# Kernel optimization log

Hardware: AMD Instinct MI355X
Metric: run time of the kernel (lower is better)

The kernel has to match this reference:

```python
import jax, jax.numpy as jnp
import numpy as np

NUM_LEARNERS = 50000
NUM_SCENES = 2000
EMBED_DIM = 128
SPARSITY = 0.1


def setup_inputs() -> dict:
    key = jax.random.key(0)
    k_m, k_w1, k_b1, k_w2, k_b2 = jax.random.split(key, 5)
    m = jax.random.uniform(k_m, (NUM_LEARNERS, NUM_SCENES), dtype=jnp.float32)
    m = jnp.where(m < SPARSITY, m, 0.0)
    return {
        "normalized_matrix": m,
        "W1": jax.random.normal(k_w1, (1, 16), dtype=jnp.float32),
        "b1": jax.random.normal(k_b1, (16,), dtype=jnp.float32),
        "W2": jax.random.normal(k_w2, (16, EMBED_DIM), dtype=jnp.float32),
        "b2": jax.random.normal(k_b2, (EMBED_DIM,), dtype=jnp.float32),
    }


def reference(normalized_matrix, W1, b1, W2, b2):
    # The torch module feeds the nonzero COLUMN INDICES (as floats) of each row
    # into MLP(1->16->d) and mean-pools. Since the MLP input is just the index j,
    # precompute mlp_out[j] for all scenes once, then a masked matmul + count
    # division gives the per-row mean over nonzero positions.
    num_scenes = normalized_matrix.shape[1]
    idx = jnp.arange(num_scenes, dtype=normalized_matrix.dtype)[:, None]  # [S, 1]
    h = jax.nn.relu(idx @ W1 + b1)                                        # [S, 16]
    mlp_out = h @ W2 + b2                                                 # [S, d]

    mask = (normalized_matrix != 0).astype(normalized_matrix.dtype)       # [L, S]
    counts = mask.sum(axis=1, keepdims=True)                              # [L, 1]
    # rows with zero nonzeros yield an all-zero mask row -> zero embedding,
    # matching the torch zeros fallback; clamp denominator to avoid 0/0.
    emb = (mask @ mlp_out) / jnp.maximum(counts, 1.0)                     # [L, d]
    return emb
```

## Files before the change

### kernel.cpp

```cpp
#include <hip/hip_runtime.h>
#include <hip/hip_fp16.h>

#define NUM_LEARNERS 50000
#define NUM_SCENES   2000
#define EMBED_DIM    128

typedef _Float16 half2v __attribute__((ext_vector_type(2)));

__global__ __launch_bounds__(256) void mlp_table_kernel(
    const float* __restrict__ W1, const float* __restrict__ b1,
    const float* __restrict__ W2, const float* __restrict__ b2,
    _Float16* __restrict__ mlp)
{
    int t = blockIdx.x * 256 + threadIdx.x;
    if (t >= NUM_SCENES * EMBED_DIM) return;
    int j = t >> 7;
    int d = t & 127;
    float x = (float)j;
    float acc = b2[d];
#pragma unroll
    for (int k = 0; k < 16; ++k) {
        float h = fmaf(x, W1[k], b1[k]);
        h = fmaxf(h, 0.0f);
        acc = fmaf(h, W2[k * EMBED_DIM + d], acc);
    }
    mlp[t] = (_Float16)acc;
}

__global__ __launch_bounds__(256) void gather_mean_kernel(
    const float* __restrict__ M, const _Float16* __restrict__ mlp,
    float* __restrict__ out)
{
    __shared__ unsigned short idxbuf[4][NUM_SCENES];
    const int  wave = threadIdx.x >> 6;
    const int  lane = threadIdx.x & 63;
    const long row  = (long)blockIdx.x * 4 + wave;

    const float4* __restrict__ M4 = (const float4*)(M + row * NUM_SCENES);
    unsigned short* myidx = idxbuf[wave];

    int count = 0;
    const unsigned long long below = (1ull << lane) - 1ull;
#pragma unroll
    for (int it = 0; it < 8; ++it) {
        int c4 = it * 64 + lane;
        float4 v = make_float4(0.f, 0.f, 0.f, 0.f);
        if (c4 < 500) v = M4[c4];
        float vals[4] = {v.x, v.y, v.z, v.w};
#pragma unroll
        for (int c = 0; c < 4; ++c) {
            bool nz = (vals[c] != 0.0f);
            unsigned long long m = __ballot(nz);
            if (nz) {
                int pos = count + __popcll(m & below);
                myidx[pos] = (unsigned short)(c4 * 4 + c);
            }
            count += __popcll(m);
        }
    }

    float ax = 0.f, ay = 0.f;
    const half2v* __restrict__ mlp2 = (const half2v*)mlp;
    const int base2 = lane;
#pragma unroll 4
    for (int n = 0; n < count; ++n) {
        int j = myidx[n];
        half2v p = mlp2[j * 64 + base2];
        ax += (float)p.x;
        ay += (float)p.y;
    }

    float inv = 1.0f / (float)(count > 0 ? count : 1);
    float2 r = make_float2(ax * inv, ay * inv);
    ((float2*)out)[row * 64 + lane] = r;
}

extern "C" void kernel_launch(void* const* d_in, const int* in_sizes, int n_in,
                              void* d_out, int out_size, void* d_ws, size_t ws_size,
                              hipStream_t stream) {
    const float* M  = (const float*)d_in[0];
    const float* W1 = (const float*)d_in[1];
    const float* b1 = (const float*)d_in[2];
    const float* W2 = (const float*)d_in[3];
    const float* b2 = (const float*)d_in[4];
    float* out = (float*)d_out;

    _Float16* mlp = (_Float16*)d_ws;

    mlp_table_kernel<<<(NUM_SCENES * EMBED_DIM + 255) / 256, 256, 0, stream>>>(
        W1, b1, W2, b2, mlp);
    gather_mean_kernel<<<NUM_LEARNERS / 4, 256, 0, stream>>>(M, mlp, out);
}
```

Before: 634.0 us.

## Pool 16-wide hidden activations before W2 instead of gathering 128-wide MLP outputs

Uses linearity of the second MLP layer: each row now sums the 16-dim ReLU hidden vectors over its nonzero columns, then applies W2 and count*b2 once per row. The per-nonzero gather shrinks from a 128-wide fp16 row to a 16-wide fp32 row, and 16 indices are processed in parallel per wave, followed by a shuffle reduction. It also switches to mbcnt for the prefix count. The kernel is likely bound by reading M (400MB), so the gain may be limited to the gather phase. A __syncthreads is added, and fp32 accumulation changes rounding slightly.

```diff
diff --git a/kernel.cpp b/kernel.cpp
--- a/kernel.cpp
+++ b/kernel.cpp
@@ -1,34 +1,24 @@
 #include <hip/hip_runtime.h>
-#include <hip/hip_fp16.h>
 
 #define NUM_LEARNERS 50000
 #define NUM_SCENES   2000
 #define EMBED_DIM    128
+#define HID          16
 
-typedef _Float16 half2v __attribute__((ext_vector_type(2)));
-
-__global__ __launch_bounds__(256) void mlp_table_kernel(
+__global__ __launch_bounds__(256) void h_table_kernel(
     const float* __restrict__ W1, const float* __restrict__ b1,
-    const float* __restrict__ W2, const float* __restrict__ b2,
-    _Float16* __restrict__ mlp)
+    float* __restrict__ htab)
 {
     int t = blockIdx.x * 256 + threadIdx.x;
-    if (t >= NUM_SCENES * EMBED_DIM) return;
-    int j = t >> 7;
-    int d = t & 127;
-    float x = (float)j;
-    float acc = b2[d];
-#pragma unroll
-    for (int k = 0; k < 16; ++k) {
-        float h = fmaf(x, W1[k], b1[k]);
-        h = fmaxf(h, 0.0f);
-        acc = fmaf(h, W2[k * EMBED_DIM + d], acc);
-    }
-    mlp[t] = (_Float16)acc;
+    if (t >= NUM_SCENES * HID) return;
+    int j = t >> 4;
+    int k = t & 15;
+    htab[t] = fmaxf(fmaf((float)j, W1[k], b1[k]), 0.0f);
 }
 
 __global__ __launch_bounds__(256) void gather_mean_kernel(
-    const float* __restrict__ M, const _Float16* __restrict__ mlp,
+    const float* __restrict__ M, const float* __restrict__ htab,
+    const float* __restrict__ W2, const float* __restrict__ b2,
     float* __restrict__ out)
 {
     __shared__ unsigned short idxbuf[4][NUM_SCENES];
@@ -40,7 +30,6 @@
     unsigned short* myidx = idxbuf[wave];
 
     int count = 0;
-    const unsigned long long below = (1ull << lane) - 1ull;
 #pragma unroll
     for (int it = 0; it < 8; ++it) {
         int c4 = it * 64 + lane;
@@ -52,27 +41,60 @@
             bool nz = (vals[c] != 0.0f);
             unsigned long long m = __ballot(nz);
             if (nz) {
-                int pos = count + __popcll(m & below);
-                myidx[pos] = (unsigned short)(c4 * 4 + c);
+                int below = __builtin_amdgcn_mbcnt_hi(
+                    (unsigned)(m >> 32),
+                    __builtin_amdgcn_mbcnt_lo((unsigned)m, 0));
+                myidx[count + below] = (unsigned short)(c4 * 4 + c);
             }
             count += __popcll(m);
         }
     }
 
-    float ax = 0.f, ay = 0.f;
-    const half2v* __restrict__ mlp2 = (const half2v*)mlp;
-    const int base2 = lane;
-#pragma unroll 4
-    for (int n = 0; n < count; ++n) {
-        int j = myidx[n];
-        half2v p = mlp2[j * 64 + base2];
-        ax += (float)p.x;
-        ay += (float)p.y;
+    __syncthreads();
+
+    const int g   = lane >> 2;
+    const int sub = lane & 3;
+    const float4* __restrict__ T4 = (const float4*)htab;
+
+    float4 acc = make_float4(0.f, 0.f, 0.f, 0.f);
+    for (int n = 0; n < count; n += 16) {
+        int i = n + g;
+        if (i < count) {
+            int j = myidx[i];
+            float4 v = T4[j * 4 + sub];
+            acc.x += v.x; acc.y += v.y; acc.z += v.z; acc.w += v.w;
+        }
     }
 
-    float inv = 1.0f / (float)(count > 0 ? count : 1);
-    float2 r = make_float2(ax * inv, ay * inv);
-    ((float2*)out)[row * 64 + lane] = r;
+#pragma unroll
+    for (int off = 4; off < 64; off <<= 1) {
+        acc.x += __shfl_xor(acc.x, off);
+        acc.y += __shfl_xor(acc.y, off);
+        acc.z += __shfl_xor(acc.z, off);
+        acc.w += __shfl_xor(acc.w, off);
+    }
+    float s[HID];
+#pragma unroll
+    for (int a = 0; a < 4; ++a) {
+        s[4 * a + 0] = __shfl(acc.x, a);
+        s[4 * a + 1] = __shfl(acc.y, a);
+        s[4 * a + 2] = __shfl(acc.z, a);
+        s[4 * a + 3] = __shfl(acc.w, a);
+    }
+
+    const float cnt = (float)count;
+    const float inv = 1.0f / fmaxf(cnt, 1.0f);
+    const float2* __restrict__ W2v = (const float2*)W2;
+    float2 bv = ((const float2*)b2)[lane];
+    float e0 = cnt * bv.x;
+    float e1 = cnt * bv.y;
+#pragma unroll
+    for (int k = 0; k < HID; ++k) {
+        float2 w = W2v[k * 64 + lane];
+        e0 = fmaf(s[k], w.x, e0);
+        e1 = fmaf(s[k], w.y, e1);
+    }
+    ((float2*)out)[row * 64 + lane] = make_float2(e0 * inv, e1 * inv);
 }
 
 extern "C" void kernel_launch(void* const* d_in, const int* in_sizes, int n_in,
@@ -85,9 +107,8 @@
     const float* b2 = (const float*)d_in[4];
     float* out = (float*)d_out;
 
-    _Float16* mlp = (_Float16*)d_ws;
+    float* htab = (float*)d_ws;
 
-    mlp_table_kernel<<<(NUM_SCENES * EMBED_DIM + 255) / 256, 256, 0, stream>>>(
-        W1, b1, W2, b2, mlp);
-    gather_mean_kernel<<<NUM_LEARNERS / 4, 256, 0, stream>>>(M, mlp, out);
+    h_table_kernel<<<(NUM_SCENES * HID + 255) / 256, 256, 0, stream>>>(W1, b1, htab);
+    gather_mean_kernel<<<NUM_LEARNERS / 4, 256, 0, stream>>>(M, htab, W2, b2, out);
 }
```

Result: faster. 564.8 us (-10.9%).

## Replace per-row sparse gather with dense masked GEMM on MFMA units

Applied to the files above, without the earlier changes.

Drops the ballot-based nonzero index compaction and the serial per-row gather of MLP table entries. Instead, each tile of the input is turned into a 0/1 fp16 mask in shared memory and multiplied against a transposed, zero-padded fp16 MLP table using 16x16x32 MFMA instructions, with register prefetch of the next K tile. Row counts are accumulated alongside and reduced with shuffles for the mean. This trades roughly ten times more arithmetic, since zeros are processed densely, for a streaming, bandwidth-bound access pattern. It also removes the latency-bound dependent loads in the gather loop.

```diff
diff --git a/kernel.cpp b/kernel.cpp
--- a/kernel.cpp
+++ b/kernel.cpp
@@ -1,78 +1,151 @@
 #include <hip/hip_runtime.h>
-#include <hip/hip_fp16.h>
 
-#define NUM_LEARNERS 50000
-#define NUM_SCENES   2000
-#define EMBED_DIM    128
+#define L  50000
+#define S  2000
+#define SP 2048
+#define D  128
+#define HID 16
+#define BM 64
+#define BK 64
+#define KITERS 32
 
-typedef _Float16 half2v __attribute__((ext_vector_type(2)));
+typedef _Float16 f16;
+typedef _Float16 half8  __attribute__((ext_vector_type(8)));
+typedef float    floatx4 __attribute__((ext_vector_type(4)));
 
-__global__ __launch_bounds__(256) void mlp_table_kernel(
+__global__ __launch_bounds__(256) void table_kernel(
     const float* __restrict__ W1, const float* __restrict__ b1,
     const float* __restrict__ W2, const float* __restrict__ b2,
-    _Float16* __restrict__ mlp)
+    f16* __restrict__ Bt)
 {
     int t = blockIdx.x * 256 + threadIdx.x;
-    if (t >= NUM_SCENES * EMBED_DIM) return;
-    int j = t >> 7;
-    int d = t & 127;
+    int d = t >> 11;
+    int j = t & 2047;
+    float acc = b2[d];
     float x = (float)j;
-    float acc = b2[d];
 #pragma unroll
-    for (int k = 0; k < 16; ++k) {
-        float h = fmaf(x, W1[k], b1[k]);
-        h = fmaxf(h, 0.0f);
-        acc = fmaf(h, W2[k * EMBED_DIM + d], acc);
+    for (int k = 0; k < HID; ++k) {
+        float h = fmaxf(fmaf(x, W1[k], b1[k]), 0.0f);
+        acc = fmaf(h, W2[k * D + d], acc);
     }
-    mlp[t] = (_Float16)acc;
+    Bt[t] = (j < S) ? (f16)acc : (f16)0.0f;
 }
 
-__global__ __launch_bounds__(256) void gather_mean_kernel(
-    const float* __restrict__ M, const _Float16* __restrict__ mlp,
+__global__ __launch_bounds__(256) void gemm_mask_kernel(
+    const float* __restrict__ M, const f16* __restrict__ Bt,
     float* __restrict__ out)
 {
-    __shared__ unsigned short idxbuf[4][NUM_SCENES];
-    const int  wave = threadIdx.x >> 6;
-    const int  lane = threadIdx.x & 63;
-    const long row  = (long)blockIdx.x * 4 + wave;
+    __shared__ f16  As[BM][72];
+    __shared__ f16  Bs[D][72];
+    __shared__ float cnt_s[BM];
 
-    const float4* __restrict__ M4 = (const float4*)(M + row * NUM_SCENES);
-    unsigned short* myidx = idxbuf[wave];
+    const int tid  = threadIdx.x;
+    const int wave = tid >> 6;
+    const int lane = tid & 63;
+    const long r0  = (long)blockIdx.x * BM;
 
-    int count = 0;
-    const unsigned long long below = (1ull << lane) - 1ull;
+    const int arow = tid >> 4;
+    const int acol = (tid & 15) * 4;
+    const int bd   = tid >> 1;
+    const int bko  = (tid & 1) * 32;
+
+    int cnt4[4] = {0, 0, 0, 0};
+    floatx4 acc[8];
 #pragma unroll
-    for (int it = 0; it < 8; ++it) {
-        int c4 = it * 64 + lane;
-        float4 v = make_float4(0.f, 0.f, 0.f, 0.f);
-        if (c4 < 500) v = M4[c4];
-        float vals[4] = {v.x, v.y, v.z, v.w};
+    for (int n = 0; n < 8; ++n) acc[n] = (floatx4){0.f, 0.f, 0.f, 0.f};
+
+    float4 av[4];
+    uint4  bv[4];
+    {
+        const int k0 = 0;
 #pragma unroll
-        for (int c = 0; c < 4; ++c) {
-            bool nz = (vals[c] != 0.0f);
-            unsigned long long m = __ballot(nz);
-            if (nz) {
-                int pos = count + __popcll(m & below);
-                myidx[pos] = (unsigned short)(c4 * 4 + c);
+        for (int p = 0; p < 4; ++p) {
+            long rg = r0 + p * 16 + arow;
+            bool ok = (rg < L);
+            av[p] = ok ? *(const float4*)(M + rg * S + k0 + acol)
+                       : make_float4(0.f, 0.f, 0.f, 0.f);
+        }
+#pragma unroll
+        for (int i = 0; i < 4; ++i)
+            bv[i] = *(const uint4*)(Bt + bd * SP + k0 + bko + i * 8);
+    }
+
+    for (int it = 0; it < KITERS; ++it) {
+        __syncthreads();
+
+#pragma unroll
+        for (int p = 0; p < 4; ++p) {
+            float4 v = av[p];
+            unsigned m0 = (v.x != 0.f) ? 0x3C00u : 0u;
+            unsigned m1 = (v.y != 0.f) ? 0x3C00u : 0u;
+            unsigned m2 = (v.z != 0.f) ? 0x3C00u : 0u;
+            unsigned m3 = (v.w != 0.f) ? 0x3C00u : 0u;
+            cnt4[p] += (v.x != 0.f) + (v.y != 0.f) + (v.z != 0.f) + (v.w != 0.f);
+            uint2 w;
+            w.x = m0 | (m1 << 16);
+            w.y = m2 | (m3 << 16);
+            *(uint2*)&As[p * 16 + arow][acol] = w;
+        }
+#pragma unroll
+        for (int i = 0; i < 4; ++i)
+            *(uint4*)&Bs[bd][bko + i * 8] = bv[i];
+
+        __syncthreads();
+
+        if (it + 1 < KITERS) {
+            const int k0 = (it + 1) * BK;
+#pragma unroll
+            for (int p = 0; p < 4; ++p) {
+                long rg = r0 + p * 16 + arow;
+                bool ok = (rg < L) && (k0 + acol < S);
+                av[p] = ok ? *(const float4*)(M + rg * S + k0 + acol)
+                           : make_float4(0.f, 0.f, 0.f, 0.f);
             }
-            count += __popcll(m);
+#pragma unroll
+            for (int i = 0; i < 4; ++i)
+                bv[i] = *(const uint4*)(Bt + bd * SP + k0 + bko + i * 8);
+        }
+
+#pragma unroll
+        for (int ks = 0; ks < 2; ++ks) {
+            half8 af = *(const half8*)&As[wave * 16 + (lane & 15)]
+                                         [(lane >> 4) * 8 + ks * 32];
+#pragma unroll
+            for (int n = 0; n < 8; ++n) {
+                half8 bf = *(const half8*)&Bs[n * 16 + (lane & 15)]
+                                             [(lane >> 4) * 8 + ks * 32];
+                acc[n] = __builtin_amdgcn_mfma_f32_16x16x32_f16(af, bf, acc[n], 0, 0, 0);
+            }
         }
     }
 
-    float ax = 0.f, ay = 0.f;
-    const half2v* __restrict__ mlp2 = (const half2v*)mlp;
-    const int base2 = lane;
-#pragma unroll 4
-    for (int n = 0; n < count; ++n) {
-        int j = myidx[n];
-        half2v p = mlp2[j * 64 + base2];
-        ax += (float)p.x;
-        ay += (float)p.y;
+#pragma unroll
+    for (int p = 0; p < 4; ++p) {
+        int c = cnt4[p];
+        c += __shfl_xor(c, 1);
+        c += __shfl_xor(c, 2);
+        c += __shfl_xor(c, 4);
+        c += __shfl_xor(c, 8);
+        if ((lane & 15) == 0)
+            cnt_s[p * 16 + wave * 4 + (lane >> 4)] = (float)c;
     }
+    __syncthreads();
 
-    float inv = 1.0f / (float)(count > 0 ? count : 1);
-    float2 r = make_float2(ax * inv, ay * inv);
-    ((float2*)out)[row * 64 + lane] = r;
+    float inv[4];
+#pragma unroll
+    for (int r = 0; r < 4; ++r) {
+        float c = cnt_s[wave * 16 + (lane >> 4) * 4 + r];
+        inv[r] = 1.0f / fmaxf(c, 1.0f);
+    }
+#pragma unroll
+    for (int n = 0; n < 8; ++n) {
+#pragma unroll
+        for (int r = 0; r < 4; ++r) {
+            long rg = r0 + wave * 16 + (lane >> 4) * 4 + r;
+            if (rg < L)
+                out[rg * D + n * 16 + (lane & 15)] = acc[n][r] * inv[r];
+        }
+    }
 }
 
 extern "C" void kernel_launch(void* const* d_in, const int* in_sizes, int n_in,
@@ -85,9 +158,8 @@
     const float* b2 = (const float*)d_in[4];
     float* out = (float*)d_out;
 
-    _Float16* mlp = (_Float16*)d_ws;
+    f16* Bt = (f16*)d_ws;
 
-    mlp_table_kernel<<<(NUM_SCENES * EMBED_DIM + 255) / 256, 256, 0, stream>>>(
-        W1, b1, W2, b2, mlp);
-    gather_mean_kernel<<<NUM_LEARNERS / 4, 256, 0, stream>>>(M, mlp, out);
+    table_kernel<<<(D * SP) / 256, 256, 0, stream>>>(W1, b1, W2, b2, Bt);
+    gemm_mask_kernel<<<(L + BM - 1) / BM, 256, 0, stream>>>(M, Bt, out);
 }
```

Result: slower. 703.2 us (+10.9%).

## Replace sparse gather-mean with dense MFMA masked GEMM against transposed table

Applied to the files above, without the earlier changes.

Replaces the per-row nonzero index compaction and gather loop with a dense masked matmul. The binary mask is built on the fly from the fp32 input as fp16 ones and multiplied against a transposed, padded fp16 MLP table using 16x16x32 MFMA instructions, with next-step A loads prefetched. This removes the ballot and LDS compaction work and the irregular gathers, but does the full dense 2000-wide reduction per row instead of only the roughly 10% nonzeros. It relies on reading the table from cache and on the input read being the dominant cost. Output stores are strided per lane and may coalesce less well.

```diff
diff --git a/kernel.cpp b/kernel.cpp
--- a/kernel.cpp
+++ b/kernel.cpp
@@ -1,78 +1,108 @@
 #include <hip/hip_runtime.h>
-#include <hip/hip_fp16.h>
 
-#define NUM_LEARNERS 50000
-#define NUM_SCENES   2000
-#define EMBED_DIM    128
+#define L  50000
+#define S  2000
+#define SP 2048
+#define D  128
+#define HID 16
+#define KSTEPS 63
 
-typedef _Float16 half2v __attribute__((ext_vector_type(2)));
+typedef _Float16 f16;
+typedef _Float16 half8  __attribute__((ext_vector_type(8)));
+typedef float    floatx4 __attribute__((ext_vector_type(4)));
 
-__global__ __launch_bounds__(256) void mlp_table_kernel(
+__global__ __launch_bounds__(256) void table_kernel(
     const float* __restrict__ W1, const float* __restrict__ b1,
     const float* __restrict__ W2, const float* __restrict__ b2,
-    _Float16* __restrict__ mlp)
+    f16* __restrict__ Bt)
 {
     int t = blockIdx.x * 256 + threadIdx.x;
-    if (t >= NUM_SCENES * EMBED_DIM) return;
-    int j = t >> 7;
-    int d = t & 127;
+    int d = t >> 11;
+    int j = t & 2047;
+    float acc = b2[d];
     float x = (float)j;
-    float acc = b2[d];
 #pragma unroll
-    for (int k = 0; k < 16; ++k) {
-        float h = fmaf(x, W1[k], b1[k]);
-        h = fmaxf(h, 0.0f);
-        acc = fmaf(h, W2[k * EMBED_DIM + d], acc);
+    for (int k = 0; k < HID; ++k) {
+        float h = fmaxf(fmaf(x, W1[k], b1[k]), 0.0f);
+        acc = fmaf(h, W2[k * D + d], acc);
     }
-    mlp[t] = (_Float16)acc;
+    Bt[t] = (j < S) ? (f16)acc : (f16)0.0f;
 }
 
-__global__ __launch_bounds__(256) void gather_mean_kernel(
-    const float* __restrict__ M, const _Float16* __restrict__ mlp,
+__global__ __launch_bounds__(256) void gemm_mask_kernel(
+    const float* __restrict__ M, const f16* __restrict__ Bt,
     float* __restrict__ out)
 {
-    __shared__ unsigned short idxbuf[4][NUM_SCENES];
     const int  wave = threadIdx.x >> 6;
     const int  lane = threadIdx.x & 63;
-    const long row  = (long)blockIdx.x * 4 + wave;
+    const int  m    = lane & 15;
+    const int  kg   = lane >> 4;
+    const long r0w  = (long)blockIdx.x * 64 + wave * 16;
+    const long rg   = r0w + m;
+    const bool rowok = (rg < L);
+    const float* __restrict__ Arow = M + (rowok ? rg : (long)(L - 1)) * S;
 
-    const float4* __restrict__ M4 = (const float4*)(M + row * NUM_SCENES);
-    unsigned short* myidx = idxbuf[wave];
+    floatx4 acc[8];
+#pragma unroll
+    for (int n = 0; n < 8; ++n) acc[n] = (floatx4){0.f, 0.f, 0.f, 0.f};
+    int cnt = 0;
 
-    int count = 0;
-    const unsigned long long below = (1ull << lane) - 1ull;
+    float4 a0 = make_float4(0.f,0.f,0.f,0.f), a1 = a0;
+    if (rowok) {
+        a0 = *(const float4*)(Arow + kg * 8);
+        a1 = *(const float4*)(Arow + kg * 8 + 4);
+    }
+
+    const f16* __restrict__ Bp = Bt + m * SP;
+
+    for (int ks = 0; ks < KSTEPS; ++ks) {
+        float4 n0 = make_float4(0.f,0.f,0.f,0.f), n1 = n0;
+        {
+            int kn = (ks + 1) * 32 + kg * 8;
+            if (rowok && kn < S) {
+                n0 = *(const float4*)(Arow + kn);
+                n1 = *(const float4*)(Arow + kn + 4);
+            }
+        }
+
+        union { half8 h; unsigned u[4]; } af;
+        unsigned b0 = (a0.x != 0.f), b1_ = (a0.y != 0.f), b2_ = (a0.z != 0.f), b3 = (a0.w != 0.f);
+        unsigned b4 = (a1.x != 0.f), b5 = (a1.y != 0.f), b6 = (a1.z != 0.f), b7 = (a1.w != 0.f);
+        af.u[0] = (b0 * 0x3C00u) | (b1_ * 0x3C000000u);
+        af.u[1] = (b2_ * 0x3C00u) | (b3 * 0x3C000000u);
+        af.u[2] = (b4 * 0x3C00u) | (b5 * 0x3C000000u);
+        af.u[3] = (b6 * 0x3C00u) | (b7 * 0x3C000000u);
+        cnt += (int)(b0 + b1_ + b2_ + b3 + b4 + b5 + b6 + b7);
+
+        const f16* bp = Bp + ks * 32 + kg * 8;
 #pragma unroll
-    for (int it = 0; it < 8; ++it) {
-        int c4 = it * 64 + lane;
-        float4 v = make_float4(0.f, 0.f, 0.f, 0.f);
-        if (c4 < 500) v = M4[c4];
-        float vals[4] = {v.x, v.y, v.z, v.w};
+        for (int nt = 0; nt < 8; ++nt) {
+            half8 bf = *(const half8*)(bp + nt * 16 * SP);
+            acc[nt] = __builtin_amdgcn_mfma_f32_16x16x32_f16(af.h, bf, acc[nt], 0, 0, 0);
+        }
+
+        a0 = n0; a1 = n1;
+    }
+
+    cnt += __shfl_xor(cnt, 16);
+    cnt += __shfl_xor(cnt, 32);
+    float cf = (float)cnt;
+
+    float inv[4];
 #pragma unroll
-        for (int c = 0; c < 4; ++c) {
-            bool nz = (vals[c] != 0.0f);
-            unsigned long long m = __ballot(nz);
-            if (nz) {
-                int pos = count + __popcll(m & below);
-                myidx[pos] = (unsigned short)(c4 * 4 + c);
-            }
-            count += __popcll(m);
+    for (int r = 0; r < 4; ++r) {
+        float c = __shfl(cf, (lane >> 4) * 4 + r);
+        inv[r] = 1.0f / fmaxf(c, 1.0f);
+    }
+#pragma unroll
+    for (int nt = 0; nt < 8; ++nt) {
+#pragma unroll
+        for (int r = 0; r < 4; ++r) {
+            long row = r0w + (lane >> 4) * 4 + r;
+            if (row < L)
+                out[row * D + nt * 16 + m] = acc[nt][r] * inv[r];
         }
     }
-
-    float ax = 0.f, ay = 0.f;
-    const half2v* __restrict__ mlp2 = (const half2v*)mlp;
-    const int base2 = lane;
-#pragma unroll 4
-    for (int n = 0; n < count; ++n) {
-        int j = myidx[n];
-        half2v p = mlp2[j * 64 + base2];
-        ax += (float)p.x;
-        ay += (float)p.y;
-    }
-
-    float inv = 1.0f / (float)(count > 0 ? count : 1);
-    float2 r = make_float2(ax * inv, ay * inv);
-    ((float2*)out)[row * 64 + lane] = r;
 }
 
 extern "C" void kernel_launch(void* const* d_in, const int* in_sizes, int n_in,
@@ -85,9 +115,8 @@
     const float* b2 = (const float*)d_in[4];
     float* out = (float*)d_out;
 
-    _Float16* mlp = (_Float16*)d_ws;
+    f16* Bt = (f16*)d_ws;
 
-    mlp_table_kernel<<<(NUM_SCENES * EMBED_DIM + 255) / 256, 256, 0, stream>>>(
-        W1, b1, W2, b2, mlp);
-    gather_mean_kernel<<<NUM_LEARNERS / 4, 256, 0, stream>>>(M, mlp, out);
+    table_kernel<<<(D * SP) / 256, 256, 0, stream>>>(W1, b1, W2, b2, Bt);
+    gemm_mask_kernel<<<(L + 63) / 64, 256, 0, stream>>>(M, Bt, out);
 }
```

Measured after the change: 734.0 us. 15.8% more time.
